# Performance work log

Measured on AMD Instinct MI355X. Metric: run time of the kernel, lower is better.

The kernel has to match this reference:

```python
import jax, jax.numpy as jnp
import numpy as np

N_AGENTS = 8
STATE_DIM = 256
NODE = 2 * N_AGENTS          # 16 graph nodes per sample
FEAT = STATE_DIM // NODE     # 16
NHID = 4
NHEADS = 4
GOUT = 2 * FEAT              # 32 = gat_output
EMBED = 32                   # mixing_embed_dim
ALPHA = 0.2                  # leaky relu slope in GAT
LAYER_IN = NODE * GOUT       # 512 = state_dim * 2
BS = 2048
T = 128


def setup_inputs() -> dict:
    key = jax.random.key(0)
    ks = jax.random.split(key, 16)
    r = lambda i, shape: jax.random.normal(ks[i], shape, dtype=jnp.float32) * 0.1
    return dict(
        agent_qs=jax.random.normal(ks[0], (BS, T, N_AGENTS), dtype=jnp.float32),
        states=jax.random.normal(ks[1], (BS, T, STATE_DIM), dtype=jnp.float32),
        # GAT params: 4 attention heads + output attention layer
        W_heads=r(2, (NHEADS, FEAT, NHID)),
        a_heads=r(3, (NHEADS, 2 * NHID, 1)),
        W_out=r(4, (NHEADS * NHID, GOUT)),
        a_out=r(5, (2 * GOUT, 1)),
        # hypernet params (torch Linear stored as [in, out])
        hw1_w=r(6, (LAYER_IN, EMBED * N_AGENTS)), hw1_b=r(7, (EMBED * N_AGENTS,)),
        hb1_w=r(8, (LAYER_IN, EMBED)), hb1_b=r(9, (EMBED,)),
        hwf_w=r(10, (LAYER_IN, EMBED)), hwf_b=r(11, (EMBED,)),
        v1_w=r(12, (LAYER_IN, EMBED)), v1_b=r(13, (EMBED,)),
        v2_w=r(14, (EMBED, 1)), v2_b=r(15, (1,)),
    )


def _gat_layer(x, W, a, concat):
    # Standard pyGAT GraphAttentionLayer; adj is all-ones so no masking needed.
    Wh = x @ W                       # [N, F']
    Fo = W.shape[1]
    e1 = Wh @ a[:Fo]                 # [N, 1]
    e2 = Wh @ a[Fo:]                 # [N, 1]
    e = jax.nn.leaky_relu(e1 + e2.T, ALPHA)  # [N, N]
    att = jax.nn.softmax(e, axis=1)
    h = att @ Wh                     # [N, F']
    return jax.nn.elu(h) if concat else h


def _gat(x, W_heads, a_heads, W_out, a_out):
    # x: [NODE, FEAT] -> [NODE, GOUT]; dropout is identity (eval mode)
    heads = jax.vmap(lambda W, a: _gat_layer(x, W, a, True))(W_heads, a_heads)  # [H, N, NHID]
    h = jnp.transpose(heads, (1, 0, 2)).reshape(x.shape[0], NHEADS * NHID)      # concat heads
    return jax.nn.elu(_gat_layer(h, W_out, a_out, False))


def reference(agent_qs, states, W_heads, a_heads, W_out, a_out,
              hw1_w, hw1_b, hb1_w, hb1_b, hwf_w, hwf_b,
              v1_w, v1_b, v2_w, v2_b):
    bs, t = agent_qs.shape[0], agent_qs.shape[1]
    nodes = states.reshape(bs * t, NODE, FEAT)
    # batched GAT over all (batch*time) tiny graphs (replaces Python loops)
    gat = jax.vmap(lambda x: _gat(x, W_heads, a_heads, W_out, a_out))(nodes)  # [bt, N, GOUT]
    s = gat.reshape(bs * t, LAYER_IN)
    qs = agent_qs.reshape(bs * t, 1, N_AGENTS)
    # QMIX mixing with hypernetworks
    w1 = jnp.abs(s @ hw1_w + hw1_b).reshape(-1, N_AGENTS, EMBED)
    b1 = (s @ hb1_w + hb1_b).reshape(-1, 1, EMBED)
    hidden = jax.nn.elu(jnp.einsum('bij,bjk->bik', qs, w1) + b1)  # [bt, 1, EMBED]
    w_final = jnp.abs(s @ hwf_w + hwf_b).reshape(-1, EMBED, 1)
    v = (jax.nn.relu(s @ v1_w + v1_b) @ v2_w + v2_b).reshape(-1, 1, 1)
    y = jnp.einsum('bij,bjk->bik', hidden, w_final) + v          # [bt, 1, 1]
    return y.reshape(bs, t, 1)
```

## Files before the change

### kernel.cpp

```cpp
#include <hip/hip_runtime.h>
#include <hip/hip_bf16.h>
#include <stdint.h>


#define BT       (2048 * 128)
#define ALPHA    0.2f
#define NTILE    22
#define KSTEPS   16
#define AUXOFF   360448

typedef __attribute__((ext_vector_type(8))) short bf16x8;
typedef __attribute__((ext_vector_type(4))) float f32x4;
typedef __attribute__((ext_vector_type(16))) float f32x16;
typedef __attribute__((ext_vector_type(2))) float f32x2;
typedef _Float16 f16x2 __attribute__((ext_vector_type(2)));

__device__ __forceinline__ f32x2 b2(float s) { return (f32x2){s, s}; }
__device__ __forceinline__ f32x2 pkfma(f32x2 a, f32x2 b, f32x2 c) {
    return __builtin_elementwise_fma(a, b, c);
}
__device__ __forceinline__ float elu1(float x) { return x > 0.f ? x : (__expf(x) - 1.f); }

__device__ __forceinline__ unsigned short f32_to_bf16_rne(float x) {
    uint32_t u = __float_as_uint(x);
    u += 0x7fffu + ((u >> 16) & 1u);
    return (unsigned short)(u >> 16);
}

__device__ __forceinline__ float fdot2f(uint32_t a, f16x2 b, float c) {
#if __has_builtin(__builtin_amdgcn_fdot2)
    return __builtin_amdgcn_fdot2(__builtin_bit_cast(f16x2, a), b, c, false);
#else
    const f16x2 av = __builtin_bit_cast(f16x2, a);
    return fmaf((float)av.x, (float)b.x, fmaf((float)av.y, (float)b.y, c));
#endif
}
__device__ __forceinline__ f16x2 pkrtz(float a, float b) {
    return __builtin_bit_cast(f16x2, __builtin_amdgcn_cvt_pkrtz(a, b));
}
__device__ __forceinline__ uint32_t cvtpk_bf16(float lo, float hi) {
    uint32_t r;
    asm("v_cvt_pk_bf16_f32 %0, %1, %2" : "=v"(r) : "v"(lo), "v"(hi));
    return r;
}
__device__ __forceinline__ f32x16 z16() {
    f32x16 r;
    #pragma unroll
    for (int i = 0; i < 16; ++i) r[i] = 0.f;
    return r;
}

__device__ __forceinline__ f32x2 softmax16p(const float* e2A, const float* e2B,
                                            f32x2 e1, f32x2* ee) {
    #pragma unroll
    for (int t4 = 0; t4 < 4; ++t4) {
        const float4 va = *(const float4*)&e2A[t4 * 4];
        const float4 vb = *(const float4*)&e2B[t4 * 4];
        const f32x2 l0 = e1 + (f32x2){va.x, vb.x};
        const f32x2 l1 = e1 + (f32x2){va.y, vb.y};
        const f32x2 l2 = e1 + (f32x2){va.z, vb.z};
        const f32x2 l3 = e1 + (f32x2){va.w, vb.w};
        ee[4*t4+0] = __builtin_elementwise_max(l0, l0 * b2(ALPHA));
        ee[4*t4+1] = __builtin_elementwise_max(l1, l1 * b2(ALPHA));
        ee[4*t4+2] = __builtin_elementwise_max(l2, l2 * b2(ALPHA));
        ee[4*t4+3] = __builtin_elementwise_max(l3, l3 * b2(ALPHA));
    }
    f32x2 m0 = __builtin_elementwise_max(ee[0], ee[1]);
    f32x2 m1 = __builtin_elementwise_max(ee[2], ee[3]);
    f32x2 m2 = __builtin_elementwise_max(ee[4], ee[5]);
    f32x2 m3 = __builtin_elementwise_max(ee[6], ee[7]);
    f32x2 m4 = __builtin_elementwise_max(ee[8], ee[9]);
    f32x2 m5 = __builtin_elementwise_max(ee[10], ee[11]);
    f32x2 m6 = __builtin_elementwise_max(ee[12], ee[13]);
    f32x2 m7 = __builtin_elementwise_max(ee[14], ee[15]);
    m0 = __builtin_elementwise_max(m0, m1); m2 = __builtin_elementwise_max(m2, m3);
    m4 = __builtin_elementwise_max(m4, m5); m6 = __builtin_elementwise_max(m6, m7);
    const f32x2 mx = __builtin_elementwise_max(__builtin_elementwise_max(m0, m2),
                                               __builtin_elementwise_max(m4, m6));
    #pragma unroll
    for (int j = 0; j < 16; ++j) {
        const f32x2 d = ee[j] - mx;
        ee[j] = (f32x2){__expf(d.x), __expf(d.y)};
    }
    f32x2 s0 = ee[0]+ee[1], s1 = ee[2]+ee[3], s2 = ee[4]+ee[5], s3 = ee[6]+ee[7];
    f32x2 s4 = ee[8]+ee[9], s5 = ee[10]+ee[11], s6 = ee[12]+ee[13], s7 = ee[14]+ee[15];
    s0 += s1; s2 += s3; s4 += s5; s6 += s7;
    const f32x2 sum = (s0 + s2) + (s4 + s6);
    return (f32x2){__builtin_amdgcn_rcpf(sum.x), __builtin_amdgcn_rcpf(sum.y)};
}

__global__ __launch_bounds__(256) void pack_b(
    const float* __restrict__ hw1_w, const float* __restrict__ hb1_w,
    const float* __restrict__ hwf_w, const float* __restrict__ v1_w,
    const float* __restrict__ W_out, const float* __restrict__ a_out,
    unsigned short* __restrict__ bpack, float* __restrict__ aux)
{
    const int gi = blockIdx.x * 256 + threadIdx.x;
    if (gi < KSTEPS * NTILE * 64) {
        const int l  = gi & 63;
        const int ni = (gi >> 6) % NTILE;
        const int kt = gi / (NTILE * 64);
        const int col = ni * 16 + (l & 15);
        const int k0  = kt * 32 + (l >> 4) * 8;
        const float* src; int stride; int c;
        if (col < 256)      { src = hw1_w; stride = 256; c = col; }
        else if (col < 288) { src = hb1_w; stride = 32;  c = col - 256; }
        else if (col < 320) { src = hwf_w; stride = 32;  c = col - 288; }
        else                { src = v1_w;  stride = 32;  c = col - 320; }
        union { unsigned short u[8]; uint4 v; } pk;
        #pragma unroll
        for (int e = 0; e < 8; ++e) {
            const int i = k0 + e;
            const int r_old = ((i & 15) << 5) + (i >> 4);
            pk.u[e] = f32_to_bf16_rne(src[(long)r_old * stride + c]);
        }
        ((uint4*)bpack)[gi] = pk.v;
    } else if (gi < KSTEPS * NTILE * 64 + 32) {
        const int a = gi - KSTEPS * NTILE * 64;
        const int which = a >> 4, f = a & 15;
        float s = 0.f;
        for (int c = 0; c < 32; ++c) s = fmaf(W_out[f * 32 + c], a_out[which * 32 + c], s);
        aux[a] = s;
    }
}

__global__ __launch_bounds__(256) void fused_kernel(
    const float* __restrict__ agent_qs, const float* __restrict__ states,
    const float* __restrict__ W_heads,  const float* __restrict__ a_heads,
    const float* __restrict__ W_out,    const float* __restrict__ a_out,
    const unsigned short* __restrict__ bpack, const float* __restrict__ aux,
    const float* __restrict__ hw1_b, const float* __restrict__ hb1_b,
    const float* __restrict__ hwf_b, const float* __restrict__ v1_b,
    const float* __restrict__ v2_w,  const float* __restrict__ v2_b,
    float* __restrict__ out)
{
    __shared__ unsigned short A[32][512];
    __shared__ float bst[384];
    __shared__ float qs[288];
    __shared__ float ysum[4][4][4];

    const int t    = threadIdx.x;
    const int w    = t >> 6;
    const int lane = t & 63;
    const int g    = lane >> 4;
    const int n    = lane & 15;
    const long sbase = (long)blockIdx.x * 32;

    char* scr = (char*)&A[0][0] + w * 8192;
    _Float16* hxA = (_Float16*)(scr + (g * 2)     * 528);
    _Float16* hxB = (_Float16*)(scr + (g * 2 + 1) * 528);
    float*    e2A = (float*)(scr + 4224 + (g * 2)     * 80);
    float*    e2B = (float*)(scr + 4224 + (g * 2 + 1) * 80);

    const int mA = w * 8 + g;
    const int mB = w * 8 + 4 + g;

    f32x2 xr2[16];
    {
        const float4* xa = (const float4*)(states + (sbase + mA) * 256 + n * 16);
        const float4* xb = (const float4*)(states + (sbase + mB) * 256 + n * 16);
        #pragma unroll
        for (int i = 0; i < 4; ++i) {
            const float4 va = xa[i], vb = xb[i];
            xr2[4*i+0] = (f32x2){va.x, vb.x};
            xr2[4*i+1] = (f32x2){va.y, vb.y};
            xr2[4*i+2] = (f32x2){va.z, vb.z};
            xr2[4*i+3] = (f32x2){va.w, vb.w};
        }
    }

    f32x2 hcat2[16];
    #pragma unroll
    for (int h = 0; h < 4; ++h) {
        f32x2 wh0 = b2(0.f), wh1 = b2(0.f), wh2 = b2(0.f), wh3 = b2(0.f);
        #pragma unroll
        for (int f = 0; f < 16; ++f) {
            const f32x2 xf = xr2[f];
            wh0 = pkfma(xf, b2(W_heads[h*64 + f*4 + 0]), wh0);
            wh1 = pkfma(xf, b2(W_heads[h*64 + f*4 + 1]), wh1);
            wh2 = pkfma(xf, b2(W_heads[h*64 + f*4 + 2]), wh2);
            wh3 = pkfma(xf, b2(W_heads[h*64 + f*4 + 3]), wh3);
        }
        const f32x2 e1 = pkfma(wh0, b2(a_heads[h*8+0]),
                         pkfma(wh1, b2(a_heads[h*8+1]),
                         pkfma(wh2, b2(a_heads[h*8+2]), wh3 * b2(a_heads[h*8+3]))));
        const f32x2 e2 = pkfma(wh0, b2(a_heads[h*8+4]),
                         pkfma(wh1, b2(a_heads[h*8+5]),
                         pkfma(wh2, b2(a_heads[h*8+6]), wh3 * b2(a_heads[h*8+7]))));
        hxA[0*16 + n] = (_Float16)wh0.x;  hxB[0*16 + n] = (_Float16)wh0.y;
        hxA[1*16 + n] = (_Float16)wh1.x;  hxB[1*16 + n] = (_Float16)wh1.y;
        hxA[2*16 + n] = (_Float16)wh2.x;  hxB[2*16 + n] = (_Float16)wh2.y;
        hxA[3*16 + n] = (_Float16)wh3.x;  hxB[3*16 + n] = (_Float16)wh3.y;
        e2A[n] = e2.x;
        e2B[n] = e2.y;

        f32x2 ee[16];
        const f32x2 inv = softmax16p(e2A, e2B, e1, ee);
        f16x2 eA[8], eB[8];
        #pragma unroll
        for (int jp = 0; jp < 8; ++jp) {
            eA[jp] = pkrtz(ee[2*jp].x, ee[2*jp+1].x);
            eB[jp] = pkrtz(ee[2*jp].y, ee[2*jp+1].y);
        }
        #pragma unroll
        for (int k = 0; k < 4; ++k) {
            const uint4 wa0 = *(const uint4*)&hxA[k*16];
            const uint4 wa1 = *(const uint4*)&hxA[k*16 + 8];
            const uint4 wb0 = *(const uint4*)&hxB[k*16];
            const uint4 wb1 = *(const uint4*)&hxB[k*16 + 8];
            float sA = 0.f, sB = 0.f;
            sA = fdot2f(wa0.x, eA[0], sA);  sB = fdot2f(wb0.x, eB[0], sB);
            sA = fdot2f(wa0.y, eA[1], sA);  sB = fdot2f(wb0.y, eB[1], sB);
            sA = fdot2f(wa0.z, eA[2], sA);  sB = fdot2f(wb0.z, eB[2], sB);
            sA = fdot2f(wa0.w, eA[3], sA);  sB = fdot2f(wb0.w, eB[3], sB);
            sA = fdot2f(wa1.x, eA[4], sA);  sB = fdot2f(wb1.x, eB[4], sB);
            sA = fdot2f(wa1.y, eA[5], sA);  sB = fdot2f(wb1.y, eB[5], sB);
            sA = fdot2f(wa1.z, eA[6], sA);  sB = fdot2f(wb1.z, eB[6], sB);
            sA = fdot2f(wa1.w, eA[7], sA);  sB = fdot2f(wb1.w, eB[7], sB);
            hcat2[h*4+k] = (f32x2){elu1(sA * inv.x), elu1(sB * inv.y)};
        }
    }

    f32x2 e1o = b2(0.f), e2o = b2(0.f);
    #pragma unroll
    for (int f = 0; f < 16; ++f) {
        e1o = pkfma(hcat2[f], b2(aux[f]), e1o);
        e2o = pkfma(hcat2[f], b2(aux[16 + f]), e2o);
    }
    e2A[n] = e2o.x;
    e2B[n] = e2o.y;
    f32x2 ee[16];
    const f32x2 invo = softmax16p(e2A, e2B, e1o, ee);
    #pragma unroll
    for (int j = 0; j < 16; ++j) ee[j] *= invo;

    {
        uint32_t hA[8], hB[8], aAv[8], aBv[8];
        #pragma unroll
        for (int p2 = 0; p2 < 8; ++p2) {
            hA[p2]  = cvtpk_bf16(hcat2[2*p2].x, hcat2[2*p2+1].x);
            hB[p2]  = cvtpk_bf16(hcat2[2*p2].y, hcat2[2*p2+1].y);
            aAv[p2] = cvtpk_bf16(ee[2*p2].x, ee[2*p2+1].x);
            aBv[p2] = cvtpk_bf16(ee[2*p2].y, ee[2*p2+1].y);
        }
        char* hb = scr + g * 1024;
        char* ab = scr + (4 + g) * 1024;
        uint4 v;
        v.x=hA[0]; v.y=hA[1]; v.z=hA[2]; v.w=hA[3];  *(uint4*)(hb + n*32)       = v;
        v.x=hA[4]; v.y=hA[5]; v.z=hA[6]; v.w=hA[7];  *(uint4*)(hb + n*32 + 16)  = v;
        v.x=hB[0]; v.y=hB[1]; v.z=hB[2]; v.w=hB[3];  *(uint4*)(hb + 512 + n*32) = v;
        v.x=hB[4]; v.y=hB[5]; v.z=hB[6]; v.w=hB[7];  *(uint4*)(hb + 512 + n*32 + 16) = v;
        v.x=aAv[0];v.y=aAv[1];v.z=aAv[2];v.w=aAv[3]; *(uint4*)(ab + n*32)       = v;
        v.x=aAv[4];v.y=aAv[5];v.z=aAv[6];v.w=aAv[7]; *(uint4*)(ab + n*32 + 16)  = v;
        v.x=aBv[0];v.y=aBv[1];v.z=aBv[2];v.w=aBv[3]; *(uint4*)(ab + 512 + n*32) = v;
        v.x=aBv[4];v.y=aBv[5];v.z=aBv[6];v.w=aBv[7]; *(uint4*)(ab + 512 + n*32 + 16) = v;
    }

    const int row  = lane & 31;
    const int half = lane >> 5;
    bf16x8 wf;
    {
        union { uint32_t d[4]; bf16x8 v; } u;
        #pragma unroll
        for (int e = 0; e < 4; ++e)
            u.d[e] = cvtpk_bf16(W_out[(half*8 + 2*e)*32 + row],
                                W_out[(half*8 + 2*e + 1)*32 + row]);
        wf = u.v;
    }

    #pragma unroll 1
    for (int gg = 0; gg < 4; ++gg) {
        const char* hb = scr + gg * 1024;
        const char* ab = scr + (4 + gg) * 1024;
        uint4 af1u = *(const uint4*)(hb + (row & 15) * 32 + (row >> 4) * 512 + half * 16);
        bf16x8 af1; memcpy(&af1, &af1u, 16);
        f32x16 D1 = __builtin_amdgcn_mfma_f32_32x32x16_bf16(af1, wf, z16(), 0, 0, 0);

        const uint32_t d0 = cvtpk_bf16(D1[0], D1[1]),   d1 = cvtpk_bf16(D1[2], D1[3]);
        const uint32_t d2 = cvtpk_bf16(D1[4], D1[5]),   d3 = cvtpk_bf16(D1[6], D1[7]);
        const uint32_t f0 = cvtpk_bf16(D1[8], D1[9]),   f1 = cvtpk_bf16(D1[10], D1[11]);
        const uint32_t f2 = cvtpk_bf16(D1[12], D1[13]), f3 = cvtpk_bf16(D1[14], D1[15]);
        const uint32_t x0 = (uint32_t)__shfl_xor((int)d0, 32);
        const uint32_t x1 = (uint32_t)__shfl_xor((int)d1, 32);
        const uint32_t x2 = (uint32_t)__shfl_xor((int)d2, 32);
        const uint32_t x3 = (uint32_t)__shfl_xor((int)d3, 32);
        const uint32_t y0 = (uint32_t)__shfl_xor((int)f0, 32);
        const uint32_t y1 = (uint32_t)__shfl_xor((int)f1, 32);
        const uint32_t y2 = (uint32_t)__shfl_xor((int)f2, 32);
        const uint32_t y3 = (uint32_t)__shfl_xor((int)f3, 32);
        union { uint32_t d[4]; bf16x8 v; } b1u, b2u;
        if (half == 0) {
            b1u.d[0]=d0; b1u.d[1]=d1; b1u.d[2]=x0; b1u.d[3]=x1;
            b2u.d[0]=f0; b2u.d[1]=f1; b2u.d[2]=y0; b2u.d[3]=y1;
        } else {
            b1u.d[0]=x2; b1u.d[1]=x3; b1u.d[2]=d2; b1u.d[3]=d3;
            b2u.d[0]=y2; b2u.d[1]=y3; b2u.d[2]=f2; b2u.d[3]=f3;
        }

        uint4 aau = {0,0,0,0}, abu = {0,0,0,0};
        if (row < 16) aau = *(const uint4*)(ab + row * 32 + half * 16);
        else          abu = *(const uint4*)(ab + 512 + (row - 16) * 32 + half * 16);
        bf16x8 aaf, abf; memcpy(&aaf, &aau, 16); memcpy(&abf, &abu, 16);
        f32x16 D2 = __builtin_amdgcn_mfma_f32_32x32x16_bf16(aaf, b1u.v, z16(), 0, 0, 0);
        D2 = __builtin_amdgcn_mfma_f32_32x32x16_bf16(abf, b2u.v, D2, 0, 0, 0);

        const int c = row;
        const int mAg = w * 8 + gg, mBg = w * 8 + 4 + gg;
        const uint32_t pA0 = cvtpk_bf16(elu1(D2[0]),  elu1(D2[1]));
        const uint32_t pA1 = cvtpk_bf16(elu1(D2[2]),  elu1(D2[3]));
        const uint32_t pA2 = cvtpk_bf16(elu1(D2[4]),  elu1(D2[5]));
        const uint32_t pA3 = cvtpk_bf16(elu1(D2[6]),  elu1(D2[7]));
        const uint32_t pB0 = cvtpk_bf16(elu1(D2[8]),  elu1(D2[9]));
        const uint32_t pB1 = cvtpk_bf16(elu1(D2[10]), elu1(D2[11]));
        const uint32_t pB2 = cvtpk_bf16(elu1(D2[12]), elu1(D2[13]));
        const uint32_t pB3 = cvtpk_bf16(elu1(D2[14]), elu1(D2[15]));
        const int u0 = 2 * c, u1 = 2 * c + 1;
        const int pa0 = (((u0 & 3) << 4) + (u0 >> 2) + mAg) & 63;
        const int pa1 = (((u1 & 3) << 4) + (u1 >> 2) + mAg) & 63;
        const int pb0 = (((u0 & 3) << 4) + (u0 >> 2) + mBg) & 63;
        const int pb1 = (((u1 & 3) << 4) + (u1 >> 2) + mBg) & 63;
        uint2 wv;
        wv.x = pA0; wv.y = pA1;
        *(uint2*)((char*)&A[0][0] + mAg * 1024 + pa0 * 16 + half * 8) = wv;
        wv.x = pA2; wv.y = pA3;
        *(uint2*)((char*)&A[0][0] + mAg * 1024 + pa1 * 16 + half * 8) = wv;
        wv.x = pB0; wv.y = pB1;
        *(uint2*)((char*)&A[0][0] + mBg * 1024 + pb0 * 16 + half * 8) = wv;
        wv.x = pB2; wv.y = pB3;
        *(uint2*)((char*)&A[0][0] + mBg * 1024 + pb1 * 16 + half * 8) = wv;
    }

    __syncthreads();

    const float bv0 = hw1_b[t];
    float bv1 = 0.f;
    if (t < 32)       bv1 = hb1_b[t];
    else if (t < 64)  bv1 = hwf_b[t - 32];
    else if (t < 96)  bv1 = v1_b[t - 64];
    else if (t < 128) bv1 = v2_w[t - 96];
    const float qv = agent_qs[sbase * 8 + t];

    const int mi  = w >> 1;
    const int pr  = w & 1;
    const int arow = mi * 16 + n;

    f32x4 acc[11];
    #pragma unroll
    for (int j = 0; j < 11; ++j) acc[j] = (f32x4){0.f, 0.f, 0.f, 0.f};

    const uint4* Bb = (const uint4*)bpack + lane;
    for (int kt = 0; kt < KSTEPS; ++kt) {
        const int chunk = (g * 16 + kt + arow) & 63;
        bf16x8 af = *(const bf16x8*)((const char*)&A[0][0] + arow * 1024 + chunk * 16);
        const uint4* bp = Bb + (kt * NTILE + pr) * 64;
        #pragma unroll
        for (int j = 0; j < 11; ++j) {
            uint4 bw = bp[(2 * j) * 64];
            bf16x8 bf;
            memcpy(&bf, &bw, 16);
            acc[j] = __builtin_amdgcn_mfma_f32_16x16x32_bf16(af, bf, acc[j], 0, 0, 0);
        }
    }

    bst[t] = bv0;
    if (t < 128) bst[256 + t] = bv1;
    qs[(t >> 3) * 9 + (t & 7)] = qv;
    __syncthreads();

    const int e = pr * 16 + n;
    float yp[4];
    #pragma unroll
    for (int r = 0; r < 4; ++r) {
        const int ms = mi * 16 + g * 4 + r;
        float hs = acc[8][r] + bst[256 + e];
        #pragma unroll
        for (int a = 0; a < 8; ++a)
            hs = fmaf(qs[ms * 9 + a], fabsf(acc[a][r] + bst[a * 32 + e]), hs);
        const float hid = elu1(hs);
        yp[r] = hid * fabsf(acc[9][r] + bst[288 + e])
              + fmaxf(acc[10][r] + bst[320 + e], 0.f) * bst[352 + e];
    }
    #pragma unroll
    for (int mask = 1; mask <= 8; mask <<= 1) {
        #pragma unroll
        for (int r = 0; r < 4; ++r) yp[r] += __shfl_xor(yp[r], mask);
    }
    if (n == 0) {
        #pragma unroll
        for (int r = 0; r < 4; ++r) ysum[w][g][r] = yp[r];
    }
    __syncthreads();

    if (t < 32) {
        const int mi2 = t >> 4, g2 = (t >> 2) & 3, r2 = t & 3;
        out[sbase + t] = ysum[mi2 * 2][g2][r2] + ysum[mi2 * 2 + 1][g2][r2] + v2_b[0];
    }
}

extern "C" void kernel_launch(void* const* d_in, const int* in_sizes, int n_in,
                              void* d_out, int out_size, void* d_ws, size_t ws_size,
                              hipStream_t stream) {
    const float* agent_qs = (const float*)d_in[0];
    const float* states   = (const float*)d_in[1];
    const float* W_heads  = (const float*)d_in[2];
    const float* a_heads  = (const float*)d_in[3];
    const float* W_out    = (const float*)d_in[4];
    const float* a_out    = (const float*)d_in[5];
    const float* hw1_w    = (const float*)d_in[6];
    const float* hw1_b    = (const float*)d_in[7];
    const float* hb1_w    = (const float*)d_in[8];
    const float* hb1_b    = (const float*)d_in[9];
    const float* hwf_w    = (const float*)d_in[10];
    const float* hwf_b    = (const float*)d_in[11];
    const float* v1_w     = (const float*)d_in[12];
    const float* v1_b     = (const float*)d_in[13];
    const float* v2_w     = (const float*)d_in[14];
    const float* v2_b     = (const float*)d_in[15];

    unsigned short* bpack = (unsigned short*)d_ws;
    float* aux = (float*)((char*)d_ws + AUXOFF);

    pack_b<<<(KSTEPS * NTILE * 64 + 32 + 255) / 256, 256, 0, stream>>>(
        hw1_w, hb1_w, hwf_w, v1_w, W_out, a_out, bpack, aux);
    fused_kernel<<<BT / 32, 256, 0, stream>>>(agent_qs, states,
                                              W_heads, a_heads, W_out, a_out,
                                              bpack, aux,
                                              hw1_b, hb1_b, hwf_b, v1_b, v2_w, v2_b,
                                              (float*)d_out);
}
```

Baseline: 293.2 us.

## Switch hypernet GEMM to 32x32x16 MFMA with LDS-staged bf16 epilogue

Replaces the 16x16x32 MFMA tiling (each wave computing 16 rows x 11 tiles) with 32x32x16 MFMA, where each wave covers all 32 samples over 2-3 column tiles of 32. The B operand is repacked to match. Accumulators are converted to bf16 and written to LDS, and a separate epilogue pass computes the mixing per (sample, embed) pair and reduces over embed through shared memory. Bias and agent_qs loads move to kernel start. The intent is to halve the redundant A-fragment and B-tile traffic per wave. The cost is extra LDS round-trips, an extra barrier, an uneven wave split (last wave does 2 tiles), and bf16 rounding of the GEMM outputs.

```diff
diff --git a/kernel.cpp b/kernel.cpp
--- a/kernel.cpp
+++ b/kernel.cpp
@@ -5,12 +5,10 @@
 
 #define BT       (2048 * 128)
 #define ALPHA    0.2f
-#define NTILE    22
-#define KSTEPS   16
+#define NTIL32   11
 #define AUXOFF   360448
 
 typedef __attribute__((ext_vector_type(8))) short bf16x8;
-typedef __attribute__((ext_vector_type(4))) float f32x4;
 typedef __attribute__((ext_vector_type(16))) float f32x16;
 typedef __attribute__((ext_vector_type(2))) float f32x2;
 typedef _Float16 f16x2 __attribute__((ext_vector_type(2)));
@@ -43,6 +41,8 @@
     asm("v_cvt_pk_bf16_f32 %0, %1, %2" : "=v"(r) : "v"(lo), "v"(hi));
     return r;
 }
+__device__ __forceinline__ float bf_lo(uint32_t u) { return __uint_as_float(u << 16); }
+__device__ __forceinline__ float bf_hi(uint32_t u) { return __uint_as_float(u & 0xffff0000u); }
 __device__ __forceinline__ f32x16 z16() {
     f32x16 r;
     #pragma unroll
@@ -96,12 +96,12 @@
     unsigned short* __restrict__ bpack, float* __restrict__ aux)
 {
     const int gi = blockIdx.x * 256 + threadIdx.x;
-    if (gi < KSTEPS * NTILE * 64) {
-        const int l  = gi & 63;
-        const int ni = (gi >> 6) % NTILE;
-        const int kt = gi / (NTILE * 64);
-        const int col = ni * 16 + (l & 15);
-        const int k0  = kt * 32 + (l >> 4) * 8;
+    if (gi < 32 * NTIL32 * 64) {
+        const int l   = gi & 63;
+        const int ti  = (gi >> 6) % NTIL32;
+        const int kt2 = gi / (NTIL32 * 64);
+        const int col = ti * 32 + (l & 31);
+        const int k0  = kt2 * 16 + (l >> 5) * 8;
         const float* src; int stride; int c;
         if (col < 256)      { src = hw1_w; stride = 256; c = col; }
         else if (col < 288) { src = hb1_w; stride = 32;  c = col - 256; }
@@ -110,13 +110,13 @@
         union { unsigned short u[8]; uint4 v; } pk;
         #pragma unroll
         for (int e = 0; e < 8; ++e) {
-            const int i = k0 + e;
-            const int r_old = ((i & 15) << 5) + (i >> 4);
+            const int k = k0 + e;
+            const int r_old = ((k & 15) << 5) + (k >> 4);
             pk.u[e] = f32_to_bf16_rne(src[(long)r_old * stride + c]);
         }
         ((uint4*)bpack)[gi] = pk.v;
-    } else if (gi < KSTEPS * NTILE * 64 + 32) {
-        const int a = gi - KSTEPS * NTILE * 64;
+    } else if (gi < 32 * NTIL32 * 64 + 32) {
+        const int a = gi - 32 * NTIL32 * 64;
         const int which = a >> 4, f = a & 15;
         float s = 0.f;
         for (int c = 0; c < 32; ++c) s = fmaf(W_out[f * 32 + c], a_out[which * 32 + c], s);
@@ -137,7 +137,7 @@
     __shared__ unsigned short A[32][512];
     __shared__ float bst[384];
     __shared__ float qs[288];
-    __shared__ float ysum[4][4][4];
+    __shared__ float cont[32][32];
 
     const int t    = threadIdx.x;
     const int w    = t >> 6;
@@ -154,6 +154,15 @@
 
     const int mA = w * 8 + g;
     const int mB = w * 8 + 4 + g;
+
+    bst[t] = hw1_b[t];
+    if (t < 32) {
+        bst[256 + t] = hb1_b[t];
+        bst[288 + t] = hwf_b[t];
+        bst[320 + t] = v1_b[t];
+        bst[352 + t] = v2_w[t];
+    }
+    qs[(t >> 3) * 9 + (t & 7)] = agent_qs[sbase * 8 + t];
 
     f32x2 xr2[16];
     {
@@ -332,68 +341,83 @@
 
     __syncthreads();
 
-    const float bv0 = hw1_b[t];
-    float bv1 = 0.f;
-    if (t < 32)       bv1 = hb1_b[t];
-    else if (t < 64)  bv1 = hwf_b[t - 32];
-    else if (t < 96)  bv1 = v1_b[t - 64];
-    else if (t < 128) bv1 = v2_w[t - 96];
-    const float qv = agent_qs[sbase * 8 + t];
-
-    const int mi  = w >> 1;
-    const int pr  = w & 1;
-    const int arow = mi * 16 + n;
-
-    f32x4 acc[11];
-    #pragma unroll
-    for (int j = 0; j < 11; ++j) acc[j] = (f32x4){0.f, 0.f, 0.f, 0.f};
-
-    const uint4* Bb = (const uint4*)bpack + lane;
-    for (int kt = 0; kt < KSTEPS; ++kt) {
-        const int chunk = (g * 16 + kt + arow) & 63;
-        bf16x8 af = *(const bf16x8*)((const char*)&A[0][0] + arow * 1024 + chunk * 16);
-        const uint4* bp = Bb + (kt * NTILE + pr) * 64;
-        #pragma unroll
-        for (int j = 0; j < 11; ++j) {
-            uint4 bw = bp[(2 * j) * 64];
-            bf16x8 bf;
-            memcpy(&bf, &bw, 16);
-            acc[j] = __builtin_amdgcn_mfma_f32_16x16x32_bf16(af, bf, acc[j], 0, 0, 0);
-        }
-    }
-
-    bst[t] = bv0;
-    if (t < 128) bst[256 + t] = bv1;
-    qs[(t >> 3) * 9 + (t & 7)] = qv;
+    const int ti0 = w * 3;
+    f32x16 acc0 = z16(), acc1 = z16(), acc2v = z16();
+
+    for (int kt2 = 0; kt2 < 32; ++kt2) {
+        const int u = 2 * kt2 + half;
+        const int phys = (((u & 3) << 4) + (u >> 2) + row) & 63;
+        uint4 au = *(const uint4*)((const char*)&A[0][0] + row * 1024 + phys * 16);
+        bf16x8 af; memcpy(&af, &au, 16);
+        const uint4* bp = (const uint4*)bpack + (kt2 * NTIL32 + ti0) * 64 + lane;
+        uint4 bw0 = bp[0];
+        uint4 bw1 = bp[64];
+        bf16x8 bf0, bf1;
+        memcpy(&bf0, &bw0, 16); memcpy(&bf1, &bw1, 16);
+        acc0 = __builtin_amdgcn_mfma_f32_32x32x16_bf16(af, bf0, acc0, 0, 0, 0);
+        acc1 = __builtin_amdgcn_mfma_f32_32x32x16_bf16(af, bf1, acc1, 0, 0, 0);
+        if (w < 3) {
+            uint4 bw2 = bp[128];
+            bf16x8 bf2; memcpy(&bf2, &bw2, 16);
+            acc2v = __builtin_amdgcn_mfma_f32_32x32x16_bf16(af, bf2, acc2v, 0, 0, 0);
+        }
+    }
+
     __syncthreads();
 
-    const int e = pr * 16 + n;
-    float yp[4];
-    #pragma unroll
-    for (int r = 0; r < 4; ++r) {
-        const int ms = mi * 16 + g * 4 + r;
-        float hs = acc[8][r] + bst[256 + e];
-        #pragma unroll
-        for (int a = 0; a < 8; ++a)
-            hs = fmaf(qs[ms * 9 + a], fabsf(acc[a][r] + bst[a * 32 + e]), hs);
-        const float hid = elu1(hs);
-        yp[r] = hid * fabsf(acc[9][r] + bst[288 + e])
-              + fmaxf(acc[10][r] + bst[320 + e], 0.f) * bst[352 + e];
-    }
-    #pragma unroll
-    for (int mask = 1; mask <= 8; mask <<= 1) {
-        #pragma unroll
-        for (int r = 0; r < 4; ++r) yp[r] += __shfl_xor(yp[r], mask);
-    }
-    if (n == 0) {
-        #pragma unroll
-        for (int r = 0; r < 4; ++r) ysum[w][g][r] = yp[r];
+    {
+        f32x16 av[3] = {acc0, acc1, acc2v};
+        const int ntj = (w < 3) ? 3 : 2;
+        #pragma unroll
+        for (int j = 0; j < 3; ++j) {
+            if (j >= ntj) break;
+            const int e = (ti0 + j) * 32 + row;
+            char* hp = (char*)&A[0][0] + e * 72;
+            #pragma unroll
+            for (int grp = 0; grp < 4; ++grp) {
+                const int m0 = grp * 8 + 4 * half;
+                uint2 v;
+                v.x = cvtpk_bf16(av[j][grp*4+0], av[j][grp*4+1]);
+                v.y = cvtpk_bf16(av[j][grp*4+2], av[j][grp*4+3]);
+                *(uint2*)(hp + m0 * 2) = v;
+            }
+        }
     }
     __syncthreads();
 
+    #pragma unroll
+    for (int it = 0; it < 2; ++it) {
+        const int slot = t + it * 256;
+        const int mp   = slot >> 5;
+        const int emb  = slot & 31;
+        const int m0   = mp * 2;
+        const char* base = (const char*)&A[0][0] + m0 * 2;
+        const uint32_t ub1 = *(const uint32_t*)(base + (256 + emb) * 72);
+        const float bb1 = bst[256 + emb];
+        float h0 = bf_lo(ub1) + bb1;
+        float h1 = bf_hi(ub1) + bb1;
+        #pragma unroll
+        for (int a = 0; a < 8; ++a) {
+            const uint32_t uw = *(const uint32_t*)(base + (a * 32 + emb) * 72);
+            const float bw_ = bst[a * 32 + emb];
+            h0 = fmaf(qs[m0 * 9 + a],       fabsf(bf_lo(uw) + bw_), h0);
+            h1 = fmaf(qs[(m0 + 1) * 9 + a], fabsf(bf_hi(uw) + bw_), h1);
+        }
+        const uint32_t uwf = *(const uint32_t*)(base + (288 + emb) * 72);
+        const uint32_t uv1 = *(const uint32_t*)(base + (320 + emb) * 72);
+        const float bwf = bst[288 + emb], bv1e = bst[320 + emb], v2we = bst[352 + emb];
+        cont[m0][emb]     = elu1(h0) * fabsf(bf_lo(uwf) + bwf)
+                          + fmaxf(bf_lo(uv1) + bv1e, 0.f) * v2we;
+        cont[m0 + 1][emb] = elu1(h1) * fabsf(bf_hi(uwf) + bwf)
+                          + fmaxf(bf_hi(uv1) + bv1e, 0.f) * v2we;
+    }
+    __syncthreads();
+
     if (t < 32) {
-        const int mi2 = t >> 4, g2 = (t >> 2) & 3, r2 = t & 3;
-        out[sbase + t] = ysum[mi2 * 2][g2][r2] + ysum[mi2 * 2 + 1][g2][r2] + v2_b[0];
+        float y = 0.f;
+        #pragma unroll
+        for (int e = 0; e < 32; ++e) y += cont[t][(t + e) & 31];
+        out[sbase + t] = y + v2_b[0];
     }
 }
 
@@ -420,7 +444,7 @@
     unsigned short* bpack = (unsigned short*)d_ws;
     float* aux = (float*)((char*)d_ws + AUXOFF);
 
-    pack_b<<<(KSTEPS * NTILE * 64 + 32 + 255) / 256, 256, 0, stream>>>(
+    pack_b<<<(32 * NTIL32 * 64 + 32 + 255) / 256, 256, 0, stream>>>(
         hw1_w, hb1_w, hwf_w, v1_w, W_out, a_out, bpack, aux);
     fused_kernel<<<BT / 32, 256, 0, stream>>>(agent_qs, states,
                                               W_heads, a_heads, W_out, a_out,
```

After: 294.3 us. Within noise of the previous version (+0.4%).
